# Performance work log

Measured on AMD Instinct MI355X. Metric: run time of the kernel, lower is better.

## Reference

```python
import jax, jax.numpy as jnp
import numpy as np

B, S, I, H = 8, 512, 512, 512
L, NH = 2, 8
N_MEM, W_MEM = 1024, 64
FF = 4 * H
HD = H // NH
# interface layout: read keys | read betas | write key | write beta | erase | write vec | write gate
D_IF = NH * W_MEM + NH + W_MEM + 1 + W_MEM + W_MEM + 1


def setup_inputs():
    key = jax.random.key(0)
    ks = jax.random.split(key, 10)
    g = lambda k, sh, s=0.02: jax.random.normal(k, sh, dtype=jnp.float32) * s
    return dict(
        x=jax.random.normal(ks[0], (B, S, I), dtype=jnp.float32),
        Wp=g(ks[1], (I, H)), bp=jnp.zeros((H,), jnp.float32),
        Wqkv=g(ks[2], (L, H, 3 * H)), bqkv=jnp.zeros((L, 3 * H), jnp.float32),
        Wo=g(ks[3], (L, H, H)), bo=jnp.zeros((L, H), jnp.float32),
        ln1_g=jnp.ones((L, H), jnp.float32), ln1_b=jnp.zeros((L, H), jnp.float32),
        W1=g(ks[4], (L, H, FF)), b1=jnp.zeros((L, FF), jnp.float32),
        W2=g(ks[5], (L, FF, H)), b2=jnp.zeros((L, H), jnp.float32),
        ln2_g=jnp.ones((L, H), jnp.float32), ln2_b=jnp.zeros((L, H), jnp.float32),
        Wi=g(ks[6], (H, D_IF)), bi=jnp.zeros((D_IF,), jnp.float32),
        M0=g(ks[7], (N_MEM, W_MEM), 0.01),
    )


def _ln(x, g, b):
    m = jnp.mean(x, -1, keepdims=True)
    v = jnp.var(x, -1, keepdims=True)
    return (x - m) * jax.lax.rsqrt(v + 1e-5) * g + b


def _encoder(h, Wqkv, bqkv, Wo, bo, ln1_g, ln1_b, W1, b1, W2, b2, ln2_g, ln2_b):
    for l in range(L):  # small fixed layer count
        qkv = h @ Wqkv[l] + bqkv[l]
        q, k, v = jnp.split(qkv, 3, axis=-1)
        to_heads = lambda t: t.reshape(B, S, NH, HD).transpose(0, 2, 1, 3)
        q, k, v = to_heads(q), to_heads(k), to_heads(v)
        att = jax.nn.softmax(jnp.einsum('bhqd,bhkd->bhqk', q, k) / np.float32(np.sqrt(HD)), -1)
        o = jnp.einsum('bhqk,bhkd->bhqd', att, v).transpose(0, 2, 1, 3).reshape(B, S, H)
        h = _ln(h + o @ Wo[l] + bo[l], ln1_g[l], ln1_b[l])
        ff = jax.nn.relu(h @ W1[l] + b1[l]) @ W2[l] + b2[l]
        h = _ln(h + ff, ln2_g[l], ln2_b[l])
    return h


def _cos_addr(M, k, beta):
    # M: [B, N, W]; k: [B, ..., W]; beta: [B, ...] -> softmax weights over N slots
    Mn = M * jax.lax.rsqrt(jnp.sum(M * M, -1, keepdims=True) + 1e-8)
    kn = k * jax.lax.rsqrt(jnp.sum(k * k, -1, keepdims=True) + 1e-8)
    sim = jnp.einsum('bnw,...w->...n', Mn, kn) if False else jnp.einsum('bnw,b...w->b...n', Mn, kn)
    return jax.nn.softmax(beta[..., None] * sim, -1)


def _dnc_memory(iface, M0):
    # iface: [B, S, D_IF]
    o = NH * W_MEM
    rk = iface[..., :o].reshape(B, S, NH, W_MEM)
    rb = jax.nn.softplus(iface[..., o:o + NH]); o += NH
    wk = iface[..., o:o + W_MEM]; o += W_MEM
    wb = jax.nn.softplus(iface[..., o]); o += 1
    er = jax.nn.sigmoid(iface[..., o:o + W_MEM]); o += W_MEM
    wv = iface[..., o:o + W_MEM]; o += W_MEM
    gw = jax.nn.sigmoid(iface[..., o])
    xs = (jnp.swapaxes(wk, 0, 1), wb.T, jnp.swapaxes(er, 0, 1),
          jnp.swapaxes(wv, 0, 1), gw.T, jnp.swapaxes(rk, 0, 1), jnp.swapaxes(rb, 0, 1))
    M_init = jnp.broadcast_to(M0, (B, N_MEM, W_MEM))

    def step(M, t):
        wk_t, wb_t, e_t, v_t, g_t, rk_t, rb_t = t
        ww = g_t[:, None] * _cos_addr(M, wk_t, wb_t)                         # [B, N]
        M = M * (1.0 - ww[:, :, None] * e_t[:, None, :]) + ww[:, :, None] * v_t[:, None, :]
        rw = _cos_addr(M, rk_t, rb_t)                                        # [B, NH, N]
        r = jnp.einsum('bhn,bnw->bhw', rw, M).reshape(B, NH * W_MEM)
        return M, r

    _, reads = jax.lax.scan(step, M_init, xs)
    return jnp.swapaxes(reads, 0, 1)  # [B, S, NH*W_MEM]


def reference(x, Wp, bp, Wqkv, bqkv, Wo, bo, ln1_g, ln1_b, W1, b1, W2, b2, ln2_g, ln2_b, Wi, bi, M0):
    h = x @ Wp + bp  # input_projection
    tout = _encoder(h, Wqkv, bqkv, Wo, bo, ln1_g, ln1_b, W1, b1, W2, b2, ln2_g, ln2_b)
    iface = tout @ Wi + bi
    read_vector = _dnc_memory(iface, M0)
    return (tout, read_vector)
```

## Files before the change

kernel.cpp:

```cpp
#include <hip/hip_runtime.h>

typedef unsigned short u16;
typedef unsigned int u32;
typedef __attribute__((ext_vector_type(8))) short s16x8;
typedef __attribute__((ext_vector_type(8))) u16 u16x8;
typedef __attribute__((ext_vector_type(4))) u16 u16x4;
typedef __attribute__((ext_vector_type(4))) u32 u32x4;
typedef __attribute__((ext_vector_type(4))) float f32x4;
typedef __attribute__((ext_vector_type(2))) float f32x2;

#define L2E 1.4426950408889634f

__device__ __forceinline__ u16 f2bf(float f) {
  unsigned u = __builtin_bit_cast(unsigned, f);
  u = (u + 0x7fffu + ((u >> 16) & 1u)) >> 16;
  return (u16)u;
}
__device__ __forceinline__ float bf2f(u16 s) {
  unsigned u = ((unsigned)s) << 16;
  return __builtin_bit_cast(float, u);
}
__device__ __forceinline__ float blo(u32 d) { return __builtin_bit_cast(float, d << 16); }
__device__ __forceinline__ float bhi(u32 d) { return __builtin_bit_cast(float, d & 0xFFFF0000u); }
__device__ __forceinline__ float sigmoidf_(float x) { return 1.f / (1.f + __expf(-x)); }
__device__ __forceinline__ float softplusf_(float x) { return (x > 20.f) ? x : logf(1.f + __expf(x)); }

__device__ __forceinline__ float wred_sum(float v) {
  #pragma unroll
  for (int d = 1; d < 64; d <<= 1) v += __shfl_xor(v, d);
  return v;
}
__device__ __forceinline__ float wred_max(float v) {
  #pragma unroll
  for (int d = 1; d < 64; d <<= 1) v = fmaxf(v, __shfl_xor(v, d));
  return v;
}

__global__ void castx_k(const float* __restrict__ in, u16* __restrict__ out, int n4) {
  int i = blockIdx.x * 256 + threadIdx.x;
  if (i < n4) {
    f32x4 v = *(const f32x4*)(in + (long)i * 4);
    u16x4 o;
    o.x = f2bf(v.x); o.y = f2bf(v.y); o.z = f2bf(v.z); o.w = f2bf(v.w);
    *(u16x4*)(out + (long)i * 4) = o;
  }
}

__global__ void castT_k(const float* __restrict__ in, u16* __restrict__ out, int K, int N) {
  long base = (long)blockIdx.z * K * N;
  int idx = blockIdx.x * 256 + threadIdx.x;
  if (idx < K * N) {
    int n = idx / K, k = idx - n * K;
    out[base + idx] = f2bf(in[base + (long)k * N + n]);
  }
}

__global__ void vtx_k(const u16* __restrict__ qkv, u16* __restrict__ vT) {
  int idx = blockIdx.x * 256 + threadIdx.x;
  int s = idx & 511;
  int d = (idx >> 9) & 63;
  int bh = idx >> 15;
  int b = bh >> 3, h = bh & 7;
  vT[idx] = qkv[((long)(b * 512 + s)) * 1536 + 1024 + h * 64 + d];
}

struct GemmP {
  const u16* A; const u16* B; const float* bias;
  float* outF; u16* outB;
  int M, N, K, lda, ldb, ldc;
  long sAb, sAh, sAz, sBb, sBh, sBz, sCb, sCh, sCz;
  int zdiv, z0;
  float alpha; int relu;
};

__global__ __launch_bounds__(256) void gemm_k(GemmP p) {
  __shared__ u16 sA[128 * 72];
  __shared__ u16 sB[128 * 72];
  int tid = threadIdx.x;
  int gp = p.z0 + blockIdx.z;
  int zb = gp / p.zdiv, zh = gp - zb * p.zdiv;
  const u16* Ab = p.A + zb * p.sAb + zh * p.sAh + (long)blockIdx.z * p.sAz + (long)blockIdx.x * 128 * p.lda;
  const u16* Bb = p.B + zb * p.sBb + zh * p.sBh + (long)blockIdx.z * p.sBz;
  long coff = zb * p.sCb + zh * p.sCh + (long)blockIdx.z * p.sCz;
  int bn = blockIdx.y * 128;
  int lane = tid & 63, wid = tid >> 6;
  int wr = wid >> 1, wc = wid & 1;

  f32x4 acc[4][4];
  f32x4 z4 = {0.f, 0.f, 0.f, 0.f};
  #pragma unroll
  for (int i = 0; i < 4; i++)
    #pragma unroll
    for (int j = 0; j < 4; j++) acc[i][j] = z4;

  int r = tid >> 1, c32 = (tid & 1) * 32;
  for (int k0 = 0; k0 < p.K; k0 += 64) {
    const u16* Ag = Ab + (long)r * p.lda + k0 + c32;
    u16x8* dA = (u16x8*)(sA + r * 72 + c32);
    #pragma unroll
    for (int i = 0; i < 4; i++) dA[i] = *(const u16x8*)(Ag + i * 8);
    int nrow = bn + r;
    u16x8* dB = (u16x8*)(sB + r * 72 + c32);
    if (nrow < p.N) {
      const u16* Bg = Bb + (long)nrow * p.ldb + k0 + c32;
      #pragma unroll
      for (int i = 0; i < 4; i++) dB[i] = *(const u16x8*)(Bg + i * 8);
    } else {
      u16x8 zz = (u16x8)0;
      #pragma unroll
      for (int i = 0; i < 4; i++) dB[i] = zz;
    }
    __syncthreads();
    #pragma unroll
    for (int ks = 0; ks < 2; ks++) {
      int ko = ks * 32 + (lane >> 4) * 8;
      s16x8 af[4], bf[4];
      #pragma unroll
      for (int m = 0; m < 4; m++) af[m] = *(const s16x8*)(sA + (wr * 64 + m * 16 + (lane & 15)) * 72 + ko);
      #pragma unroll
      for (int n = 0; n < 4; n++) bf[n] = *(const s16x8*)(sB + (wc * 64 + n * 16 + (lane & 15)) * 72 + ko);
      #pragma unroll
      for (int m = 0; m < 4; m++)
        #pragma unroll
        for (int n = 0; n < 4; n++)
          acc[m][n] = __builtin_amdgcn_mfma_f32_16x16x32_bf16(af[m], bf[n], acc[m][n], 0, 0, 0);
    }
    __syncthreads();
  }

  int row0 = blockIdx.x * 128 + wr * 64;
  int col0 = bn + wc * 64;
  #pragma unroll
  for (int n = 0; n < 4; n++) {
    int col = col0 + n * 16 + (lane & 15);
    if (col >= p.N) continue;
    float bv = p.bias ? p.bias[col] : 0.f;
    #pragma unroll
    for (int m = 0; m < 4; m++) {
      #pragma unroll
      for (int q = 0; q < 4; q++) {
        int row = row0 + m * 16 + (lane >> 4) * 4 + q;
        float v = acc[m][n][q] * p.alpha + bv;
        if (p.relu) v = fmaxf(v, 0.f);
        long ci = coff + (long)row * p.ldc + col;
        if (p.outF) p.outF[ci] = v;
        if (p.outB) p.outB[ci] = f2bf(v);
      }
    }
  }
}

__global__ __launch_bounds__(64) void ln_k(const float* __restrict__ a, const float* __restrict__ res,
                                           const float* __restrict__ g, const float* __restrict__ bb,
                                           float* __restrict__ outF, u16* __restrict__ outB) {
  int row = blockIdx.x, t = threadIdx.x;
  const float* ar = a + (long)row * 512;
  const float* rr = res + (long)row * 512;
  float x[8];
  float s1 = 0.f;
  #pragma unroll
  for (int i = 0; i < 8; i++) { x[i] = ar[i * 64 + t] + rr[i * 64 + t]; s1 += x[i]; }
  s1 = wred_sum(s1);
  float mean = s1 * (1.f / 512.f);
  float s2 = 0.f;
  #pragma unroll
  for (int i = 0; i < 8; i++) { float d = x[i] - mean; s2 += d * d; }
  s2 = wred_sum(s2);
  float inv = rsqrtf(s2 * (1.f / 512.f) + 1e-5f);
  #pragma unroll
  for (int i = 0; i < 8; i++) {
    int cc = i * 64 + t;
    float y = (x[i] - mean) * inv * g[cc] + bb[cc];
    outF[(long)row * 512 + cc] = y;
    outB[(long)row * 512 + cc] = f2bf(y);
  }
}

__global__ __launch_bounds__(64) void smaxb_k(u16* __restrict__ p) {
  long row = blockIdx.x;
  u16* pr = p + row * 512;
  int t = threadIdx.x;
  u16x8 v = *(const u16x8*)(pr + t * 8);
  float f[8];
  float mx = -1e30f;
  #pragma unroll
  for (int i = 0; i < 8; i++) { f[i] = bf2f(v[i]); mx = fmaxf(mx, f[i]); }
  mx = wred_max(mx);
  float se = 0.f;
  #pragma unroll
  for (int i = 0; i < 8; i++) { f[i] = __expf(f[i] - mx); se += f[i]; }
  se = wred_sum(se);
  float inv = __builtin_amdgcn_rcpf(se);
  #pragma unroll
  for (int i = 0; i < 8; i++) v[i] = f2bf(f[i] * inv);
  *(u16x8*)(pr + t * 8) = v;
}

__global__ __launch_bounds__(256) void prep_k(const float* __restrict__ iface,
                                              float* __restrict__ rec) {
  int idx = blockIdx.x * 4 + (threadIdx.x >> 6);
  int lane = threadIdx.x & 63;
  const float* r = iface + (long)idx * 714;
  float* o = rec + (long)idx * 712;
  float wk = r[520 + lane];
  float s2k = wred_sum(wk * wk);
  float wb = softplusf_(r[584]);
  o[lane] = wk * (wb * L2E * rsqrtf(s2k + 1e-8f));
  o[64 + lane] = sigmoidf_(r[585 + lane]);
  o[128 + lane] = r[649 + lane];
  #pragma unroll
  for (int h = 0; h < 8; h++) {
    float rk = r[h * 64 + lane];
    float s2r = wred_sum(rk * rk);
    float rb = softplusf_(r[512 + h]);
    o[192 + h * 64 + lane] = rk * (rb * L2E * rsqrtf(s2r + 1e-8f));
  }
  if (!lane) o[704] = sigmoidf_(r[713]);
}

__global__ __launch_bounds__(1024, 4) void scan1_k(const float* __restrict__ rec,
                                                   const float* __restrict__ M0,
                                                   float* __restrict__ ww_out,
                                                   u16* __restrict__ snap) {
  int b = blockIdx.x, tid = threadIdx.x, lane = tid & 63, wid = tid >> 6;
  __shared__ float s_red[2][16];
  f32x4 m[16];
  {
    const float* M0r = M0 + (long)tid * 64;
    #pragma unroll
    for (int i = 0; i < 16; i++) m[i] = *(const f32x4*)(M0r + i * 4);
  }
  const float* rb_ = rec + (long)b * 512 * 712;
  float* wwb = ww_out + (long)b * 512 * 1024;
  u16* snb = snap + (long)b * 2097152;

  for (int t = 0; t < 512; ++t) {
    const float* kr = rb_ + (long)t * 712;
    if ((t & 15) == 0) {
      u16* sr = snb + ((long)(t >> 4) * 1024 + tid) * 64;
      #pragma unroll
      for (int i = 0; i < 8; i++) {
        u16x8 o;
        #pragma unroll
        for (int j = 0; j < 8; j++) { int e = i * 8 + j; o[j] = f2bf(m[e >> 2][e & 3]); }
        *(u16x8*)(sr + i * 8) = o;
      }
    }
    f32x4 n4 = {1e-8f, 0.f, 0.f, 0.f};
    f32x4 d4 = {0.f, 0.f, 0.f, 0.f};
    #pragma unroll
    for (int i = 0; i < 16; i++) {
      f32x4 kv = *(const f32x4*)(kr + i * 4);
      f32x4 mv = m[i];
      n4.x = __builtin_fmaf(mv.x, mv.x, n4.x); n4.y = __builtin_fmaf(mv.y, mv.y, n4.y);
      n4.z = __builtin_fmaf(mv.z, mv.z, n4.z); n4.w = __builtin_fmaf(mv.w, mv.w, n4.w);
      d4.x = __builtin_fmaf(kv.x, mv.x, d4.x); d4.y = __builtin_fmaf(kv.y, mv.y, d4.y);
      d4.z = __builtin_fmaf(kv.z, mv.z, d4.z); d4.w = __builtin_fmaf(kv.w, mv.w, d4.w);
    }
    float n2 = (n4.x + n4.y) + (n4.z + n4.w);
    float dot = (d4.x + d4.y) + (d4.z + d4.w);
    float ew = __builtin_amdgcn_exp2f(dot * rsqrtf(n2));
    float ssum = wred_sum(ew);
    if (!lane) s_red[t & 1][wid] = ssum;
    __syncthreads();
    float tot;
    {
      const f32x4* rr = (const f32x4*)&s_red[t & 1][0];
      f32x4 a = rr[0], bq = rr[1], cq = rr[2], dq = rr[3];
      tot = ((a.x + a.y) + (a.z + a.w)) + ((bq.x + bq.y) + (bq.z + bq.w)) +
            ((cq.x + cq.y) + (cq.z + cq.w)) + ((dq.x + dq.y) + (dq.z + dq.w));
    }
    float ww = kr[704] * ew * __builtin_amdgcn_rcpf(tot);
    wwb[(long)t * 1024 + tid] = ww;

    #pragma unroll
    for (int i = 0; i < 16; i++) {
      f32x4 ev = *(const f32x4*)(kr + 64 + i * 4);
      f32x4 vv = *(const f32x4*)(kr + 128 + i * 4);
      f32x4 mv = m[i];
      float t0 = vv.x - ev.x * mv.x;
      float t1 = vv.y - ev.y * mv.y;
      float t2 = vv.z - ev.z * mv.z;
      float t3 = vv.w - ev.w * mv.w;
      mv.x = __builtin_fmaf(ww, t0, mv.x);
      mv.y = __builtin_fmaf(ww, t1, mv.y);
      mv.z = __builtin_fmaf(ww, t2, mv.z);
      mv.w = __builtin_fmaf(ww, t3, mv.w);
      m[i] = mv;
    }
  }
}

#define P2_LDS 148480
__global__ __launch_bounds__(1024, 4) void scan2_k(const float* __restrict__ rec,
                                                   const float* __restrict__ ww_in,
                                                   const u16* __restrict__ snap,
                                                   float* __restrict__ out) {
  int b = blockIdx.x, c = blockIdx.y, tid = threadIdx.x, lane = tid & 63, wid = tid >> 6;
  extern __shared__ char smem[];
  u16* s_Mbf = (u16*)smem;
  u16* s_rw = s_Mbf + 65536;
  float* s_red = (float*)(s_rw + 8192);

  f32x4 m[16];
  {
    const u16* sr = snap + (((long)b * 32 + c) * 1024 + tid) * 64;
    #pragma unroll
    for (int i = 0; i < 8; i++) {
      u16x8 v = *(const u16x8*)(sr + i * 8);
      #pragma unroll
      for (int j = 0; j < 8; j++) { int e = i * 8 + j; m[e >> 2][e & 3] = bf2f(v[j]); }
    }
  }
  const float* rb_ = rec + (long)b * 512 * 712;
  const float* wwb = ww_in + (long)b * 512 * 1024;
  float* outb = out + (long)b * 512 * 512;
  int t0 = c * 16;
  int n7 = tid & 7;
  int blkswz = tid ^ ((tid >> 3) & 7);

  for (int ti = 0; ti < 16; ++ti) {
    int t = t0 + ti, cb = ti & 1;
    const float* kr = rb_ + (long)t * 712;
    float ww = wwb[(long)t * 1024 + tid];
    __syncthreads();

    f32x4 n4 = {1e-8f, 0.f, 0.f, 0.f};
    #pragma unroll
    for (int i = 0; i < 16; i++) {
      f32x4 ev = *(const f32x4*)(kr + 64 + i * 4);
      f32x4 vv = *(const f32x4*)(kr + 128 + i * 4);
      f32x4 mv = m[i];
      float u0 = vv.x - ev.x * mv.x;
      float u1 = vv.y - ev.y * mv.y;
      float u2 = vv.z - ev.z * mv.z;
      float u3 = vv.w - ev.w * mv.w;
      mv.x = __builtin_fmaf(ww, u0, mv.x);
      mv.y = __builtin_fmaf(ww, u1, mv.y);
      mv.z = __builtin_fmaf(ww, u2, mv.z);
      mv.w = __builtin_fmaf(ww, u3, mv.w);
      m[i] = mv;
      n4.x = __builtin_fmaf(mv.x, mv.x, n4.x); n4.y = __builtin_fmaf(mv.y, mv.y, n4.y);
      n4.z = __builtin_fmaf(mv.z, mv.z, n4.z); n4.w = __builtin_fmaf(mv.w, mv.w, n4.w);
    }
    float invm = rsqrtf((n4.x + n4.y) + (n4.z + n4.w));
    #pragma unroll
    for (int i = 0; i < 8; i++) {
      u16x8 o;
      #pragma unroll
      for (int j = 0; j < 8; j++) { int e = i * 8 + j; o[j] = f2bf(m[e >> 2][e & 3]); }
      *(u16x8*)(s_Mbf + tid * 64 + ((i ^ n7) << 3)) = o;
    }
    float eh[8];
    u16x8 ehb;
    #pragma unroll
    for (int h = 0; h < 8; h++) {
      f32x4 a = {0.f, 0.f, 0.f, 0.f};
      #pragma unroll
      for (int i = 0; i < 16; i++) {
        f32x4 kv = *(const f32x4*)(kr + 192 + h * 64 + i * 4);
        f32x4 mv = m[i];
        a.x = __builtin_fmaf(kv.x, mv.x, a.x); a.y = __builtin_fmaf(kv.y, mv.y, a.y);
        a.z = __builtin_fmaf(kv.z, mv.z, a.z); a.w = __builtin_fmaf(kv.w, mv.w, a.w);
      }
      float d = (a.x + a.y) + (a.z + a.w);
      eh[h] = __builtin_amdgcn_exp2f(d * invm);
      ehb[h] = f2bf(eh[h]);
    }
    *(u16x8*)(s_rw + (blkswz << 3)) = ehb;
    #pragma unroll
    for (int h = 0; h < 8; h++) {
      float sh = wred_sum(eh[h]);
      if (!lane) s_red[cb * 128 + wid * 8 + h] = sh;
    }
    __syncthreads();

    float p[8];
    #pragma unroll
    for (int h = 0; h < 8; h++) p[h] = 0.f;
    int rbase = wid << 6;
    int cblk = lane >> 3, cin = lane & 7;
    #pragma unroll 4
    for (int j = 0; j < 64; j++) {
      int r = rbase + j;
      float mf = bf2f(s_Mbf[(r << 6) + (((cblk ^ r) & 7) << 3) + cin]);
      int rsw = r ^ ((r >> 3) & 7);
      u32x4 rr = *(const u32x4*)(s_rw + (rsw << 3));
      p[0] = __builtin_fmaf(mf, blo(rr.x), p[0]); p[1] = __builtin_fmaf(mf, bhi(rr.x), p[1]);
      p[2] = __builtin_fmaf(mf, blo(rr.y), p[2]); p[3] = __builtin_fmaf(mf, bhi(rr.y), p[3]);
      p[4] = __builtin_fmaf(mf, blo(rr.z), p[4]); p[5] = __builtin_fmaf(mf, bhi(rr.z), p[5]);
      p[6] = __builtin_fmaf(mf, blo(rr.w), p[6]); p[7] = __builtin_fmaf(mf, bhi(rr.w), p[7]);
    }
    {
      float* pb = (float*)(s_Mbf + (wid << 12));
      #pragma unroll
      for (int h = 0; h < 8; h++) pb[h * 64 + lane] = p[h];
    }
    __syncthreads();

    if (tid < 512) {
      int h = tid >> 6, ow = tid & 63;
      float s = 0.f;
      #pragma unroll
      for (int j = 0; j < 16; j++) s += ((const float*)(s_Mbf + (j << 12)))[h * 64 + ow];
      float tt = 0.f;
      #pragma unroll
      for (int j = 0; j < 16; j++) tt += s_red[cb * 128 + j * 8 + h];
      outb[(long)t * 512 + tid] = s * __builtin_amdgcn_rcpf(tt);
    }
  }
}

static void launch_gemm(hipStream_t stream, const u16* A, int lda, const u16* B, int ldb,
                        const float* bias, float* oF, u16* oB, int ldc,
                        int M, int N, int K, int gz,
                        long sAb, long sAh, long sAz, long sBb, long sBh, long sBz,
                        long sCb, long sCh, long sCz, int zdiv, int z0, float alpha, int relu) {
  GemmP p;
  p.A = A; p.B = B; p.bias = bias; p.outF = oF; p.outB = oB;
  p.M = M; p.N = N; p.K = K; p.lda = lda; p.ldb = ldb; p.ldc = ldc;
  p.sAb = sAb; p.sAh = sAh; p.sAz = sAz;
  p.sBb = sBb; p.sBh = sBh; p.sBz = sBz;
  p.sCb = sCb; p.sCh = sCh; p.sCz = sCz;
  p.zdiv = zdiv; p.z0 = z0; p.alpha = alpha; p.relu = relu;
  dim3 g(M / 128, (N + 127) / 128, gz);
  gemm_k<<<g, 256, 0, stream>>>(p);
}

extern "C" void kernel_launch(void* const* d_in, const int* in_sizes, int n_in,
                              void* d_out, int out_size, void* d_ws, size_t ws_size,
                              hipStream_t stream) {
  (void)in_sizes; (void)n_in; (void)out_size; (void)ws_size;
  const float* x    = (const float*)d_in[0];
  const float* Wp   = (const float*)d_in[1];
  const float* bp   = (const float*)d_in[2];
  const float* Wqkv = (const float*)d_in[3];
  const float* bqkv = (const float*)d_in[4];
  const float* Wo   = (const float*)d_in[5];
  const float* bo   = (const float*)d_in[6];
  const float* ln1g = (const float*)d_in[7];
  const float* ln1b = (const float*)d_in[8];
  const float* W1   = (const float*)d_in[9];
  const float* b1   = (const float*)d_in[10];
  const float* W2   = (const float*)d_in[11];
  const float* b2   = (const float*)d_in[12];
  const float* ln2g = (const float*)d_in[13];
  const float* ln2b = (const float*)d_in[14];
  const float* Wi   = (const float*)d_in[15];
  const float* bi   = (const float*)d_in[16];
  const float* M0   = (const float*)d_in[17];
  float* outF = (float*)d_out;

  char* ws = (char*)d_ws;
  u16* WpT   = (u16*)ws;
  u16* WqkvT = WpT + 262144;
  u16* WoT   = WqkvT + 1572864;
  u16* W1T   = WoT + 524288;
  u16* W2T   = W1T + 2097152;
  u16* WiT   = W2T + 2097152;
  u16* xb    = WiT + 365568;
  u16* hb    = xb + 2097152;
  float* h   = (float*)(hb + 2097152);
  u16* qkvb  = (u16*)(h + 2097152);
  u16* vT    = qkvb + 6291456;
  float* scores = (float*)(vT + 2097152);
  u16* pbuf  = (u16*)(scores + 4194304);
  u16* obuf  = pbuf + 4194304;
  float* gout = (float*)(obuf + 2097152);
  u16* ffb   = (u16*)(gout + 2924544);
  float* ifbuf = (float*)(ffb + 8388608);
  u16* scoresB = (u16*)gout;
  float* prepb = (float*)qkvb;
  float* wwbuf = scores;
  u16* snapb  = pbuf;

  castx_k<<<2048, 256, 0, stream>>>(x, xb, 524288);
  castT_k<<<dim3(1024, 1, 1), 256, 0, stream>>>(Wp, WpT, 512, 512);
  castT_k<<<dim3(3072, 1, 2), 256, 0, stream>>>(Wqkv, WqkvT, 512, 1536);
  castT_k<<<dim3(1024, 1, 2), 256, 0, stream>>>(Wo, WoT, 512, 512);
  castT_k<<<dim3(4096, 1, 2), 256, 0, stream>>>(W1, W1T, 512, 2048);
  castT_k<<<dim3(4096, 1, 2), 256, 0, stream>>>(W2, W2T, 2048, 512);
  castT_k<<<dim3(1428, 1, 1), 256, 0, stream>>>(Wi, WiT, 512, 714);

  launch_gemm(stream, xb, 512, WpT, 512, bp, h, hb, 512, 4096, 512, 512,
              1, 0,0,0, 0,0,0, 0,0,0, 1, 0, 1.f, 0);

  for (int l = 0; l < 2; ++l) {
    launch_gemm(stream, hb, 512, WqkvT + (long)l * 786432, 512, bqkv + l * 1536,
                nullptr, qkvb, 1536, 4096, 1536, 512,
                1, 0,0,0, 0,0,0, 0,0,0, 1, 0, 1.f, 0);
    vtx_k<<<8192, 256, 0, stream>>>(qkvb, vT);
    launch_gemm(stream, qkvb, 1536, qkvb + 512, 1536, nullptr, nullptr, scoresB, 512,
                512, 512, 64, 64,
                786432, 64, 0,  786432, 64, 0,  2097152, 262144, 0, 8, 0, 0.125f, 0);
    smaxb_k<<<32768, 64, 0, stream>>>(scoresB);
    launch_gemm(stream, scoresB, 512, vT, 512, nullptr, nullptr, obuf, 512,
                512, 64, 512, 64,
                2097152, 262144, 0,  262144, 32768, 0,  262144, 64, 0, 8, 0, 1.f, 0);
    launch_gemm(stream, obuf, 512, WoT + (long)l * 262144, 512, bo + l * 512,
                gout, nullptr, 512, 4096, 512, 512,
                1, 0,0,0, 0,0,0, 0,0,0, 1, 0, 1.f, 0);
    ln_k<<<4096, 64, 0, stream>>>(gout, h, ln1g + l * 512, ln1b + l * 512, h, hb);
    launch_gemm(stream, hb, 512, W1T + (long)l * 1048576, 512, b1 + l * 2048,
                nullptr, ffb, 2048, 4096, 2048, 512,
                1, 0,0,0, 0,0,0, 0,0,0, 1, 0, 1.f, 1);
    launch_gemm(stream, ffb, 2048, W2T + (long)l * 1048576, 2048, b2 + l * 512,
                gout, nullptr, 512, 4096, 512, 2048,
                1, 0,0,0, 0,0,0, 0,0,0, 1, 0, 1.f, 0);
    float* lnout = (l == 1) ? outF : h;
    ln_k<<<4096, 64, 0, stream>>>(gout, h, ln2g + l * 512, ln2b + l * 512, lnout, hb);
  }

  launch_gemm(stream, hb, 512, WiT, 512, bi, ifbuf, nullptr, 714,
              4096, 714, 512, 1, 0,0,0, 0,0,0, 0,0,0, 1, 0, 1.f, 0);

  prep_k<<<1024, 256, 0, stream>>>(ifbuf, prepb);
  scan1_k<<<8, 1024, 0, stream>>>(prepb, M0, wwbuf, snapb);
  hipFuncSetAttribute(reinterpret_cast<const void*>(scan2_k),
                      hipFuncAttributeMaxDynamicSharedMemorySize, P2_LDS);
  scan2_k<<<dim3(8, 32), 1024, P2_LDS, stream>>>(prepb, wwbuf, snapb, outF + 2097152);
}
```

Measured before the change: 2.612 ms.

## Split scan1 memory rows across four blocks with cross-block softmax sync

Each batch's sequential write-addressing scan moves from one 1024-thread block to four 256-thread blocks, each owning 256 memory rows. Every time step combines the per-block softmax partial sums through global atomics with spin-wait polling. A memset zeroes the partial buffer before launch. The aim is to spread the serial scan over more CUs and shorten the in-block barriers. The cost is a global-memory handshake on each of the 512 steps, which depends on all 32 blocks being resident together and on a partial sum never being exactly zero.

```diff
diff --git a/kernel.cpp b/kernel.cpp
--- a/kernel.cpp
+++ b/kernel.cpp
@@ -218,26 +218,32 @@
   if (!lane) o[704] = sigmoidf_(r[713]);
 }
 
-__global__ __launch_bounds__(1024, 4) void scan1_k(const float* __restrict__ rec,
-                                                   const float* __restrict__ M0,
-                                                   float* __restrict__ ww_out,
-                                                   u16* __restrict__ snap) {
-  int b = blockIdx.x, tid = threadIdx.x, lane = tid & 63, wid = tid >> 6;
-  __shared__ float s_red[2][16];
+__global__ __launch_bounds__(256, 1) void scan1_k(const float* __restrict__ rec,
+                                                  const float* __restrict__ M0,
+                                                  float* __restrict__ ww_out,
+                                                  u16* __restrict__ snap,
+                                                  float* __restrict__ part) {
+  int bg = blockIdx.x;
+  int b = bg >> 2, g = bg & 3;
+  int tid = threadIdx.x, lane = tid & 63, wid = tid >> 6;
+  int row = g * 256 + tid;
+  __shared__ float s_red[4];
+  __shared__ float s_tot;
   f32x4 m[16];
   {
-    const float* M0r = M0 + (long)tid * 64;
+    const float* M0r = M0 + (long)row * 64;
     #pragma unroll
     for (int i = 0; i < 16; i++) m[i] = *(const f32x4*)(M0r + i * 4);
   }
   const float* rb_ = rec + (long)b * 512 * 712;
   float* wwb = ww_out + (long)b * 512 * 1024;
   u16* snb = snap + (long)b * 2097152;
+  float* pb = part + (long)b * 512 * 4;
 
   for (int t = 0; t < 512; ++t) {
     const float* kr = rb_ + (long)t * 712;
     if ((t & 15) == 0) {
-      u16* sr = snb + ((long)(t >> 4) * 1024 + tid) * 64;
+      u16* sr = snb + ((long)(t >> 4) * 1024 + row) * 64;
       #pragma unroll
       for (int i = 0; i < 8; i++) {
         u16x8 o;
@@ -261,17 +267,28 @@
     float dot = (d4.x + d4.y) + (d4.z + d4.w);
     float ew = __builtin_amdgcn_exp2f(dot * rsqrtf(n2));
     float ssum = wred_sum(ew);
-    if (!lane) s_red[t & 1][wid] = ssum;
-    __syncthreads();
-    float tot;
-    {
-      const f32x4* rr = (const f32x4*)&s_red[t & 1][0];
-      f32x4 a = rr[0], bq = rr[1], cq = rr[2], dq = rr[3];
-      tot = ((a.x + a.y) + (a.z + a.w)) + ((bq.x + bq.y) + (bq.z + bq.w)) +
-            ((cq.x + cq.y) + (cq.z + cq.w)) + ((dq.x + dq.y) + (dq.z + dq.w));
-    }
-    float ww = kr[704] * ew * __builtin_amdgcn_rcpf(tot);
-    wwb[(long)t * 1024 + tid] = ww;
+    if (!lane) s_red[wid] = ssum;
+    __syncthreads();
+    if (tid == 0) {
+      float bs = (s_red[0] + s_red[1]) + (s_red[2] + s_red[3]);
+      float* ps = pb + t * 4;
+      __hip_atomic_store(ps + g, bs, __ATOMIC_RELEASE, __HIP_MEMORY_SCOPE_AGENT);
+      float acc = bs;
+      #pragma unroll
+      for (int gg = 0; gg < 4; gg++) {
+        if (gg == g) continue;
+        float v = __hip_atomic_load(ps + gg, __ATOMIC_ACQUIRE, __HIP_MEMORY_SCOPE_AGENT);
+        while (v == 0.f) {
+          __builtin_amdgcn_s_sleep(1);
+          v = __hip_atomic_load(ps + gg, __ATOMIC_ACQUIRE, __HIP_MEMORY_SCOPE_AGENT);
+        }
+        acc += v;
+      }
+      s_tot = __builtin_amdgcn_rcpf(acc);
+    }
+    __syncthreads();
+    float ww = kr[704] * ew * s_tot;
+    wwb[(long)t * 1024 + row] = ww;
 
     #pragma unroll
     for (int i = 0; i < 16; i++) {
@@ -392,9 +409,9 @@
       p[6] = __builtin_fmaf(mf, blo(rr.w), p[6]); p[7] = __builtin_fmaf(mf, bhi(rr.w), p[7]);
     }
     {
-      float* pb = (float*)(s_Mbf + (wid << 12));
-      #pragma unroll
-      for (int h = 0; h < 8; h++) pb[h * 64 + lane] = p[h];
+      float* pbw = (float*)(s_Mbf + (wid << 12));
+      #pragma unroll
+      for (int h = 0; h < 8; h++) pbw[h * 64 + lane] = p[h];
     }
     __syncthreads();
 
@@ -473,6 +490,7 @@
   float* prepb = (float*)qkvb;
   float* wwbuf = scores;
   u16* snapb  = pbuf;
+  float* partb = (float*)vT;
 
   castx_k<<<2048, 256, 0, stream>>>(x, xb, 524288);
   castT_k<<<dim3(1024, 1, 1), 256, 0, stream>>>(Wp, WpT, 512, 512);
@@ -515,7 +533,8 @@
               4096, 714, 512, 1, 0,0,0, 0,0,0, 0,0,0, 1, 0, 1.f, 0);
 
   prep_k<<<1024, 256, 0, stream>>>(ifbuf, prepb);
-  scan1_k<<<8, 1024, 0, stream>>>(prepb, M0, wwbuf, snapb);
+  hipMemsetAsync(partb, 0, 8 * 512 * 4 * sizeof(float), stream);
+  scan1_k<<<32, 256, 0, stream>>>(prepb, M0, wwbuf, snapb, partb);
   hipFuncSetAttribute(reinterpret_cast<const void*>(scan2_k),
                       hipFuncAttributeMaxDynamicSharedMemorySize, P2_LDS);
   scan2_k<<<dim3(8, 32), 1024, P2_LDS, stream>>>(prepb, wwbuf, snapb, outF + 2097152);
```

Measured after the change: 3.020 ms. 1.16x slower.
